# Optimization experiments

Measured on AMD Instinct MI355X. Metric: run time of the kernel, lower is better.

Reference implementation:

```python
import jax, jax.numpy as jnp
import numpy as np

N, E, NFEAT, NHID = 50000, 800000, 256, 128
EPS = 1e-5


def setup_inputs() -> dict:
    key = jax.random.key(0)
    ks = jax.random.split(key, 12)
    s = 0.05
    return {
        "x": jax.random.normal(ks[0], (N, NFEAT), jnp.float32),
        "adj": jax.random.randint(ks[1], (2, E), 0, N, jnp.int32),
        "features": jax.random.uniform(ks[2], (E,), jnp.float32),
        "W_in": jax.random.normal(ks[3], (NHID, NFEAT), jnp.float32) * s,
        "b_in": jnp.zeros((NHID,), jnp.float32),
        "W1_rel": jax.random.normal(ks[4], (NHID, NHID), jnp.float32) * s,
        "b1_rel": jnp.zeros((NHID,), jnp.float32),
        "W1_root": jax.random.normal(ks[5], (NHID, NHID), jnp.float32) * s,
        "W2_rel": jax.random.normal(ks[6], (NHID, NHID), jnp.float32) * s,
        "b2_rel": jnp.zeros((NHID,), jnp.float32),
        "W2_root": jax.random.normal(ks[7], (NHID, NHID), jnp.float32) * s,
        "gamma": jnp.ones((NHID,), jnp.float32),
        "beta": jnp.zeros((NHID,), jnp.float32),
    }


def _graph_conv(h, src, dst, ew, W_rel, b_rel, W_root):
    # torch_geometric GraphConv (aggr='add'):
    #   out_i = W_rel @ (sum_{j->i} e_ji * h_j) + b_rel + W_root @ h_i
    msg = h[src] * ew[:, None]                       # [E, NHID] gather
    agg = jax.ops.segment_sum(msg, dst, num_segments=N)  # [N, NHID] scatter-add
    return agg @ W_rel.T + b_rel + h @ W_root.T


def _batch_norm(h, gamma, beta):
    mu = h.mean(axis=0)
    var = h.var(axis=0)
    return (h - mu) * jax.lax.rsqrt(var + EPS) * gamma + beta


def reference(x, adj, features, W_in, b_in, W1_rel, b1_rel, W1_root,
              W2_rel, b2_rel, W2_root, gamma, beta):
    src, dst = adj[0], adj[1]
    h = jax.nn.relu(x @ W_in.T + b_in)               # linear_in + relu (dropout=identity in eval)
    h = _graph_conv(h, src, dst, features, W1_rel, b1_rel, W1_root)
    h = jax.nn.relu(_batch_norm(h, gamma, beta))     # batch1 + relu
    h = _graph_conv(h, src, dst, features, W2_rel, b2_rel, W2_root)
    return _batch_norm(h, gamma, beta)               # batch1 reused (per source)
```

## Files before the change

### kernel.cpp

```cpp
#include <hip/hip_runtime.h>
#include <hip/hip_bf16.h>

#define NNODES 50000
#define NEDGES 800000
#define NF 256
#define NH 128
#define BN_EPS 1e-5f
#define MTILES (NNODES / 16)
#define GEMM_BLOCKS 512
#define NBUCKETS 196
#define BCAP 4608
#define SCAT_BLOCKS ((NEDGES + 2047) / 2048)

typedef __attribute__((ext_vector_type(8))) __bf16 bf16x8;
typedef __attribute__((ext_vector_type(4))) float floatx4;

__device__ __forceinline__ __hip_bfloat16 f2bf(float f) { return __float2bfloat16(f); }
__device__ __forceinline__ float bits2f(unsigned short b) {
    union { unsigned u; float f; } u; u.u = ((unsigned)b) << 16; return u.f;
}

__device__ __forceinline__ bf16x8 cvt8(const float* __restrict__ p) {
    floatx4 a0 = *(const floatx4*)p;
    floatx4 a1 = *(const floatx4*)(p + 4);
    bf16x8 r;
    r[0] = (__bf16)a0[0]; r[1] = (__bf16)a0[1]; r[2] = (__bf16)a0[2]; r[3] = (__bf16)a0[3];
    r[4] = (__bf16)a1[0]; r[5] = (__bf16)a1[1]; r[6] = (__bf16)a1[2]; r[7] = (__bf16)a1[3];
    return r;
}

__global__ __launch_bounds__(256) void convert_w_kernel(
    const float* __restrict__ W_in, const float* __restrict__ W1r,
    const float* __restrict__ W1o, const float* __restrict__ W2r,
    const float* __restrict__ W2o, __hip_bfloat16* __restrict__ wbf,
    int* __restrict__ gcursor, float* __restrict__ st1, float* __restrict__ st2)
{
    const int i = blockIdx.x * 256 + threadIdx.x;
    if (blockIdx.x == 0 && threadIdx.x < NBUCKETS)
        gcursor[threadIdx.x] = threadIdx.x * BCAP;
    if (blockIdx.x == 1) { st1[threadIdx.x] = 0.f; st2[threadIdx.x] = 0.f; }
    const float* src; int off;
    if (i < 32768)      { src = W_in; off = i; }
    else if (i < 49152) { src = W1r;  off = i - 32768; }
    else if (i < 65536) { src = W1o;  off = i - 49152; }
    else if (i < 81920) { src = W2r;  off = i - 65536; }
    else                { src = W2o;  off = i - 81920; }
    wbf[i] = f2bf(src[off]);
}

__global__ __launch_bounds__(256) void bucket_scatter_kernel(
    const int* __restrict__ adj, const float* __restrict__ ew,
    int* __restrict__ gcursor, uint2* __restrict__ pairbuf,
    unsigned char* __restrict__ nodebuf)
{
    __shared__ int cnt[NBUCKETS];
    __shared__ int base[NBUCKETS];
    const int tid = threadIdx.x;
    if (tid < NBUCKETS) cnt[tid] = 0;
    __syncthreads();
    const int e0 = blockIdx.x * 2048;
    #pragma unroll
    for (int i = 0; i < 8; ++i) {
        const int e = e0 + i * 256 + tid;
        if (e < NEDGES) atomicAdd(&cnt[adj[NEDGES + e] >> 8], 1);
    }
    __syncthreads();
    if (tid < NBUCKETS) {
        base[tid] = atomicAdd(&gcursor[tid], cnt[tid]);
        cnt[tid] = 0;
    }
    __syncthreads();
    #pragma unroll
    for (int i = 0; i < 8; ++i) {
        const int e = e0 + i * 256 + tid;
        if (e >= NEDGES) continue;
        const int dst = adj[NEDGES + e];
        const int b = dst >> 8;
        const int off = atomicAdd(&cnt[b], 1);
        const int slot = base[b] + off;
        if (slot < (b + 1) * BCAP) {
            pairbuf[slot] = make_uint2((unsigned)adj[e], __float_as_uint(ew[e]));
            nodebuf[slot] = (unsigned char)(dst & 255);
        }
    }
}

__global__ __launch_bounds__(256) void bucket_sort_kernel(
    const int* __restrict__ gcursor, const uint2* __restrict__ pairbuf,
    const unsigned char* __restrict__ nodebuf, uint2* __restrict__ sorted,
    int* __restrict__ rowptr, int* __restrict__ rowend)
{
    const int b = blockIdx.x;
    const int tid = threadIdx.x;
    const int capbase = b * BCAP;
    int n = gcursor[b] - capbase;
    if (n > BCAP) n = BCAP;

    __shared__ int cnt[256];
    __shared__ int s[256];
    cnt[tid] = 0;
    __syncthreads();
    for (int j = tid; j < n; j += 256)
        atomicAdd(&cnt[nodebuf[capbase + j]], 1);
    __syncthreads();
    const int v = cnt[tid];
    s[tid] = v;
    __syncthreads();
    for (int off = 1; off < 256; off <<= 1) {
        const int t = (tid >= off) ? s[tid - off] : 0;
        __syncthreads();
        s[tid] += t;
        __syncthreads();
    }
    const int excl = s[tid] - v;
    const int node = b * 256 + tid;
    if (node < NNODES) {
        rowptr[node] = capbase + excl;
        rowend[node] = capbase + excl + v;
    }
    cnt[tid] = excl;
    __syncthreads();
    for (int j = tid; j < n; j += 256) {
        const int nd = nodebuf[capbase + j];
        const int pos = atomicAdd(&cnt[nd], 1);
        sorted[capbase + pos] = pairbuf[capbase + j];
    }
}

__global__ __launch_bounds__(256, 2) void gemm_in_kernel(
    const float* __restrict__ X, const __hip_bfloat16* __restrict__ W,
    const float* __restrict__ bias, __hip_bfloat16* __restrict__ out)
{
    const int waveG = blockIdx.x * 4 + (threadIdx.x >> 6);
    const int lane = threadIdx.x & 63;
    const int half = waveG & 1;
    const int ar = lane & 15;
    const int q  = lane >> 4;

    bf16x8 bw[4][8];
    float bv[4];
    #pragma unroll
    for (int t = 0; t < 4; ++t) {
        const int row = half * 64 + t * 16 + ar;
        bv[t] = bias[row];
        #pragma unroll
        for (int k = 0; k < 8; ++k)
            bw[t][k] = *(const bf16x8*)(W + (size_t)row * NF + k * 32 + q * 8);
    }

    for (int strip = waveG >> 1; strip < MTILES; strip += GEMM_BLOCKS * 2) {
        const int m0 = strip << 4;
        floatx4 acc[4] = {};
        #pragma unroll
        for (int k = 0; k < 8; ++k) {
            const bf16x8 a = cvt8(X + (size_t)(m0 + ar) * NF + k * 32 + q * 8);
            #pragma unroll
            for (int t = 0; t < 4; ++t)
                acc[t] = __builtin_amdgcn_mfma_f32_16x16x32_bf16(a, bw[t][k], acc[t], 0, 0, 0);
        }
        #pragma unroll
        for (int t = 0; t < 4; ++t) {
            const int col = half * 64 + t * 16 + ar;
            #pragma unroll
            for (int r = 0; r < 4; ++r) {
                const float v = fmaxf(acc[t][r] + bv[t], 0.f);
                out[(size_t)(m0 + q * 4 + r) * NH + col] = f2bf(v);
            }
        }
    }
}

__global__ __launch_bounds__(256) void gather_kernel(
    const uint2* __restrict__ sorted, const int* __restrict__ rowptr,
    const int* __restrict__ rowend,
    const __hip_bfloat16* __restrict__ h, __hip_bfloat16* __restrict__ agg)
{
    const int node = blockIdx.x * 4 + (threadIdx.x >> 6);
    if (node >= NNODES) return;
    const int lane = threadIdx.x & 63;
    const int beg = rowptr[node];
    const int end = rowend[node];
    const unsigned short* hb = (const unsigned short*)h;

    float a0[8] = {}, a1[8] = {};

    int j = beg;
    if ((j & 1) && j < end) {
        const uint2 ev = sorted[j++];
        const float w = __uint_as_float(ev.y);
        const unsigned raw = *(const unsigned*)(hb + (size_t)ev.x * NH + lane * 2);
        a0[0] += w * bits2f((unsigned short)(raw & 0xffffu));
        a1[0] += w * bits2f((unsigned short)(raw >> 16));
    }
    for (; j + 8 <= end; j += 8) {
        const uint4 e01 = *(const uint4*)(sorted + j);
        const uint4 e23 = *(const uint4*)(sorted + j + 2);
        const uint4 e45 = *(const uint4*)(sorted + j + 4);
        const uint4 e67 = *(const uint4*)(sorted + j + 6);
        const unsigned r0 = *(const unsigned*)(hb + (size_t)e01.x * NH + lane * 2);
        const unsigned r1 = *(const unsigned*)(hb + (size_t)e01.z * NH + lane * 2);
        const unsigned r2 = *(const unsigned*)(hb + (size_t)e23.x * NH + lane * 2);
        const unsigned r3 = *(const unsigned*)(hb + (size_t)e23.z * NH + lane * 2);
        const unsigned r4 = *(const unsigned*)(hb + (size_t)e45.x * NH + lane * 2);
        const unsigned r5 = *(const unsigned*)(hb + (size_t)e45.z * NH + lane * 2);
        const unsigned r6 = *(const unsigned*)(hb + (size_t)e67.x * NH + lane * 2);
        const unsigned r7 = *(const unsigned*)(hb + (size_t)e67.z * NH + lane * 2);
        const float w0 = __uint_as_float(e01.y), w1 = __uint_as_float(e01.w);
        const float w2 = __uint_as_float(e23.y), w3 = __uint_as_float(e23.w);
        const float w4 = __uint_as_float(e45.y), w5 = __uint_as_float(e45.w);
        const float w6 = __uint_as_float(e67.y), w7 = __uint_as_float(e67.w);
        a0[0] += w0 * bits2f((unsigned short)(r0 & 0xffffu));
        a1[0] += w0 * bits2f((unsigned short)(r0 >> 16));
        a0[1] += w1 * bits2f((unsigned short)(r1 & 0xffffu));
        a1[1] += w1 * bits2f((unsigned short)(r1 >> 16));
        a0[2] += w2 * bits2f((unsigned short)(r2 & 0xffffu));
        a1[2] += w2 * bits2f((unsigned short)(r2 >> 16));
        a0[3] += w3 * bits2f((unsigned short)(r3 & 0xffffu));
        a1[3] += w3 * bits2f((unsigned short)(r3 >> 16));
        a0[4] += w4 * bits2f((unsigned short)(r4 & 0xffffu));
        a1[4] += w4 * bits2f((unsigned short)(r4 >> 16));
        a0[5] += w5 * bits2f((unsigned short)(r5 & 0xffffu));
        a1[5] += w5 * bits2f((unsigned short)(r5 >> 16));
        a0[6] += w6 * bits2f((unsigned short)(r6 & 0xffffu));
        a1[6] += w6 * bits2f((unsigned short)(r6 >> 16));
        a0[7] += w7 * bits2f((unsigned short)(r7 & 0xffffu));
        a1[7] += w7 * bits2f((unsigned short)(r7 >> 16));
    }
    for (; j + 2 <= end; j += 2) {
        const uint4 e01 = *(const uint4*)(sorted + j);
        const unsigned r0 = *(const unsigned*)(hb + (size_t)e01.x * NH + lane * 2);
        const unsigned r1 = *(const unsigned*)(hb + (size_t)e01.z * NH + lane * 2);
        const float w0 = __uint_as_float(e01.y), w1 = __uint_as_float(e01.w);
        a0[0] += w0 * bits2f((unsigned short)(r0 & 0xffffu));
        a1[0] += w0 * bits2f((unsigned short)(r0 >> 16));
        a0[1] += w1 * bits2f((unsigned short)(r1 & 0xffffu));
        a1[1] += w1 * bits2f((unsigned short)(r1 >> 16));
    }
    if (j < end) {
        const uint2 ev = sorted[j];
        const float w = __uint_as_float(ev.y);
        const unsigned raw = *(const unsigned*)(hb + (size_t)ev.x * NH + lane * 2);
        a0[0] += w * bits2f((unsigned short)(raw & 0xffffu));
        a1[0] += w * bits2f((unsigned short)(raw >> 16));
    }
    const float f0 = ((a0[0] + a0[1]) + (a0[2] + a0[3])) + ((a0[4] + a0[5]) + (a0[6] + a0[7]));
    const float f1 = ((a1[0] + a1[1]) + (a1[2] + a1[3])) + ((a1[4] + a1[5]) + (a1[6] + a1[7]));
    unsigned o = ((unsigned)__bfloat16_as_ushort(f2bf(f1)) << 16) |
                 (unsigned)__bfloat16_as_ushort(f2bf(f0));
    *(unsigned*)((unsigned short*)agg + (size_t)node * NH + lane * 2) = o;
}

__global__ __launch_bounds__(256, 2) void gemm_conv_kernel(
    const __hip_bfloat16* __restrict__ agg, const __hip_bfloat16* __restrict__ h,
    const __hip_bfloat16* __restrict__ Wrel, const __hip_bfloat16* __restrict__ Wroot,
    const float* __restrict__ bias, float* __restrict__ out,
    float* __restrict__ stats)
{
    const int waveG = blockIdx.x * 4 + (threadIdx.x >> 6);
    const int lane = threadIdx.x & 63;
    const int half = waveG & 1;
    const int ar = lane & 15;
    const int q  = lane >> 4;

    bf16x8 brel[4][4], brt[4][4];
    float bv[4];
    #pragma unroll
    for (int t = 0; t < 4; ++t) {
        const int row = half * 64 + t * 16 + ar;
        bv[t] = bias[row];
        #pragma unroll
        for (int k = 0; k < 4; ++k) {
            brel[t][k] = *(const bf16x8*)(Wrel + (size_t)row * NH + k * 32 + q * 8);
            brt[t][k]  = *(const bf16x8*)(Wroot + (size_t)row * NH + k * 32 + q * 8);
        }
    }

    float s1[4] = {}, s2[4] = {};

    for (int strip = waveG >> 1; strip < MTILES; strip += GEMM_BLOCKS * 2) {
        const int m0 = strip << 4;
        floatx4 acc[4] = {};
        #pragma unroll
        for (int k = 0; k < 4; ++k) {
            const bf16x8 a = *(const bf16x8*)(agg + (size_t)(m0 + ar) * NH + k * 32 + q * 8);
            #pragma unroll
            for (int t = 0; t < 4; ++t)
                acc[t] = __builtin_amdgcn_mfma_f32_16x16x32_bf16(a, brel[t][k], acc[t], 0, 0, 0);
        }
        #pragma unroll
        for (int k = 0; k < 4; ++k) {
            const bf16x8 a = *(const bf16x8*)(h + (size_t)(m0 + ar) * NH + k * 32 + q * 8);
            #pragma unroll
            for (int t = 0; t < 4; ++t)
                acc[t] = __builtin_amdgcn_mfma_f32_16x16x32_bf16(a, brt[t][k], acc[t], 0, 0, 0);
        }
        #pragma unroll
        for (int t = 0; t < 4; ++t) {
            const int col = half * 64 + t * 16 + ar;
            #pragma unroll
            for (int r = 0; r < 4; ++r) {
                const float v = acc[t][r] + bv[t];
                out[(size_t)(m0 + q * 4 + r) * NH + col] = v;
                s1[t] += v; s2[t] += v * v;
            }
        }
    }

    __shared__ float sst[256];
    sst[threadIdx.x] = 0.f;
    __syncthreads();
    #pragma unroll
    for (int t = 0; t < 4; ++t) {
        float a = s1[t], b = s2[t];
        a += __shfl_xor(a, 16, 64); a += __shfl_xor(a, 32, 64);
        b += __shfl_xor(b, 16, 64); b += __shfl_xor(b, 32, 64);
        if (q == 0) {
            const int col = half * 64 + t * 16 + ar;
            atomicAdd(&sst[col], a);
            atomicAdd(&sst[128 + col], b);
        }
    }
    __syncthreads();
    unsafeAtomicAdd(&stats[threadIdx.x], sst[threadIdx.x]);
}

__global__ __launch_bounds__(256) void bn_relu_bf16_kernel(
    const float* __restrict__ t, const float* __restrict__ stats,
    const float* __restrict__ gamma, const float* __restrict__ beta,
    __hip_bfloat16* __restrict__ out)
{
    const size_t i = (size_t)blockIdx.x * blockDim.x + threadIdx.x;
    const int c = (int)(i & (NH - 1));
    const float inv_n = 1.0f / (float)NNODES;
    const float mu = stats[c] * inv_n;
    const float var = stats[128 + c] * inv_n - mu * mu;
    const float rs = rsqrtf(var + BN_EPS);
    float v = (t[i] - mu) * rs * gamma[c] + beta[c];
    out[i] = f2bf(fmaxf(v, 0.f));
}

__global__ __launch_bounds__(256) void bn_f32_kernel(
    const float* __restrict__ t, const float* __restrict__ stats,
    const float* __restrict__ gamma, const float* __restrict__ beta,
    float* __restrict__ out)
{
    const size_t i = (size_t)blockIdx.x * blockDim.x + threadIdx.x;
    const int c = (int)(i & (NH - 1));
    const float inv_n = 1.0f / (float)NNODES;
    const float mu = stats[c] * inv_n;
    const float var = stats[128 + c] * inv_n - mu * mu;
    const float rs = rsqrtf(var + BN_EPS);
    out[i] = (t[i] - mu) * rs * gamma[c] + beta[c];
}


extern "C" void kernel_launch(void* const* d_in, const int* in_sizes, int n_in,
                              void* d_out, int out_size, void* d_ws, size_t ws_size,
                              hipStream_t stream)
{
    const float* x    = (const float*)d_in[0];
    const int*   adj  = (const int*)d_in[1];
    const float* ew   = (const float*)d_in[2];
    const float* W_in = (const float*)d_in[3];
    const float* b_in = (const float*)d_in[4];
    const float* W1r  = (const float*)d_in[5];
    const float* b1   = (const float*)d_in[6];
    const float* W1o  = (const float*)d_in[7];
    const float* W2r  = (const float*)d_in[8];
    const float* b2   = (const float*)d_in[9];
    const float* W2o  = (const float*)d_in[10];
    const float* gmm  = (const float*)d_in[11];
    const float* bta  = (const float*)d_in[12];
    float* out = (float*)d_out;
    float* t   = (float*)d_out;

    char* ws = (char*)d_ws;
    __hip_bfloat16* h0  = (__hip_bfloat16*)ws; ws += (size_t)NNODES * NH * 2;
    __hip_bfloat16* h1  = (__hip_bfloat16*)ws; ws += (size_t)NNODES * NH * 2;
    __hip_bfloat16* agg = (__hip_bfloat16*)ws; ws += (size_t)NNODES * NH * 2;
    uint2*          sorted  = (uint2*)ws;      ws += (size_t)NBUCKETS * BCAP * 8;
    uint2*          pairbuf = (uint2*)ws;      ws += (size_t)NBUCKETS * BCAP * 8;
    unsigned char*  nodebuf = (unsigned char*)ws; ws += (size_t)NBUCKETS * BCAP;
    int*            rowptr  = (int*)ws;        ws += NNODES * 4;
    int*            rowend  = (int*)ws;        ws += NNODES * 4;
    int*            gcursor = (int*)ws;        ws += ((NBUCKETS + 3) & ~3) * 4;
    __hip_bfloat16* wbf     = (__hip_bfloat16*)ws; ws += 98304 * 2;
    float*          st1     = (float*)ws;      ws += 256 * 4;
    float*          st2     = (float*)ws;      ws += 256 * 4;

    const __hip_bfloat16* Wb_in = wbf;
    const __hip_bfloat16* Wb1r  = wbf + 32768;
    const __hip_bfloat16* Wb1o  = wbf + 49152;
    const __hip_bfloat16* Wb2r  = wbf + 65536;
    const __hip_bfloat16* Wb2o  = wbf + 81920;

    const int node_blocks = (NNODES + 3) / 4;
    const int bn_blocks   = (NNODES * NH) / 256;

    convert_w_kernel<<<98304 / 256, 256, 0, stream>>>(W_in, W1r, W1o, W2r, W2o,
                                                      wbf, gcursor, st1, st2);
    bucket_scatter_kernel<<<SCAT_BLOCKS, 256, 0, stream>>>(adj, ew, gcursor, pairbuf, nodebuf);
    bucket_sort_kernel<<<NBUCKETS, 256, 0, stream>>>(gcursor, pairbuf, nodebuf,
                                                     sorted, rowptr, rowend);

    gemm_in_kernel<<<GEMM_BLOCKS, 256, 0, stream>>>(x, Wb_in, b_in, h0);
    gather_kernel<<<node_blocks, 256, 0, stream>>>(sorted, rowptr, rowend, h0, agg);
    gemm_conv_kernel<<<GEMM_BLOCKS, 256, 0, stream>>>(agg, h0, Wb1r, Wb1o, b1, t, st1);
    bn_relu_bf16_kernel<<<bn_blocks, 256, 0, stream>>>(t, st1, gmm, bta, h1);

    gather_kernel<<<node_blocks, 256, 0, stream>>>(sorted, rowptr, rowend, h1, agg);
    gemm_conv_kernel<<<GEMM_BLOCKS, 256, 0, stream>>>(agg, h1, Wb2r, Wb2o, b2, t, st2);
    bn_f32_kernel<<<bn_blocks, 256, 0, stream>>>(t, st2, gmm, bta, out);
}
```

Baseline: 327.0 us.

## Fuse bucket scatter with input GEMM, retile GEMMs, store pre-BN output in bf16

Merges the edge bucket-scatter kernel and the input linear GEMM into one launch, with extra blocks taking the GEMM role so the two independent stages can run concurrently. Both GEMM kernels are retiled so each block's four waves split the 128 output columns of a single 16-row strip (32 columns per wave). This halves the weight registers each wave holds and the launch bounds are raised to 4 blocks per CU. The pre-batchnorm conv output is now written to a bf16 workspace buffer instead of fp32 in the output buffer, halving that traffic at some cost in precision before the final normalization.

```diff
diff --git a/kernel.cpp b/kernel.cpp
--- a/kernel.cpp
+++ b/kernel.cpp
@@ -48,39 +48,80 @@
     wbf[i] = f2bf(src[off]);
 }
 
-__global__ __launch_bounds__(256) void bucket_scatter_kernel(
+__global__ __launch_bounds__(256, 4) void scatter_gemm_in_kernel(
     const int* __restrict__ adj, const float* __restrict__ ew,
     int* __restrict__ gcursor, uint2* __restrict__ pairbuf,
-    unsigned char* __restrict__ nodebuf)
+    unsigned char* __restrict__ nodebuf,
+    const float* __restrict__ X, const __hip_bfloat16* __restrict__ W,
+    const float* __restrict__ bias, __hip_bfloat16* __restrict__ out)
 {
     __shared__ int cnt[NBUCKETS];
     __shared__ int base[NBUCKETS];
     const int tid = threadIdx.x;
-    if (tid < NBUCKETS) cnt[tid] = 0;
-    __syncthreads();
-    const int e0 = blockIdx.x * 2048;
-    #pragma unroll
-    for (int i = 0; i < 8; ++i) {
-        const int e = e0 + i * 256 + tid;
-        if (e < NEDGES) atomicAdd(&cnt[adj[NEDGES + e] >> 8], 1);
-    }
-    __syncthreads();
-    if (tid < NBUCKETS) {
-        base[tid] = atomicAdd(&gcursor[tid], cnt[tid]);
-        cnt[tid] = 0;
-    }
-    __syncthreads();
-    #pragma unroll
-    for (int i = 0; i < 8; ++i) {
-        const int e = e0 + i * 256 + tid;
-        if (e >= NEDGES) continue;
-        const int dst = adj[NEDGES + e];
-        const int b = dst >> 8;
-        const int off = atomicAdd(&cnt[b], 1);
-        const int slot = base[b] + off;
-        if (slot < (b + 1) * BCAP) {
-            pairbuf[slot] = make_uint2((unsigned)adj[e], __float_as_uint(ew[e]));
-            nodebuf[slot] = (unsigned char)(dst & 255);
+
+    if (blockIdx.x < SCAT_BLOCKS) {
+        if (tid < NBUCKETS) cnt[tid] = 0;
+        __syncthreads();
+        const int e0 = blockIdx.x * 2048;
+        #pragma unroll
+        for (int i = 0; i < 8; ++i) {
+            const int e = e0 + i * 256 + tid;
+            if (e < NEDGES) atomicAdd(&cnt[adj[NEDGES + e] >> 8], 1);
+        }
+        __syncthreads();
+        if (tid < NBUCKETS) {
+            base[tid] = atomicAdd(&gcursor[tid], cnt[tid]);
+            cnt[tid] = 0;
+        }
+        __syncthreads();
+        #pragma unroll
+        for (int i = 0; i < 8; ++i) {
+            const int e = e0 + i * 256 + tid;
+            if (e >= NEDGES) continue;
+            const int dst = adj[NEDGES + e];
+            const int b = dst >> 8;
+            const int off = atomicAdd(&cnt[b], 1);
+            const int slot = base[b] + off;
+            if (slot < (b + 1) * BCAP) {
+                pairbuf[slot] = make_uint2((unsigned)adj[e], __float_as_uint(ew[e]));
+                nodebuf[slot] = (unsigned char)(dst & 255);
+            }
+        }
+    } else {
+        const int q4   = tid >> 6;
+        const int lane = tid & 63;
+        const int ar = lane & 15;
+        const int q  = lane >> 4;
+
+        bf16x8 bw[2][8];
+        float bv[2];
+        #pragma unroll
+        for (int tt = 0; tt < 2; ++tt) {
+            const int row = q4 * 32 + tt * 16 + ar;
+            bv[tt] = bias[row];
+            #pragma unroll
+            for (int k = 0; k < 8; ++k)
+                bw[tt][k] = *(const bf16x8*)(W + (size_t)row * NF + k * 32 + q * 8);
+        }
+
+        for (int s = blockIdx.x - SCAT_BLOCKS; s < MTILES; s += GEMM_BLOCKS) {
+            const int m0 = s << 4;
+            floatx4 acc[2] = {};
+            #pragma unroll
+            for (int k = 0; k < 8; ++k) {
+                const bf16x8 a = cvt8(X + (size_t)(m0 + ar) * NF + k * 32 + q * 8);
+                acc[0] = __builtin_amdgcn_mfma_f32_16x16x32_bf16(a, bw[0][k], acc[0], 0, 0, 0);
+                acc[1] = __builtin_amdgcn_mfma_f32_16x16x32_bf16(a, bw[1][k], acc[1], 0, 0, 0);
+            }
+            #pragma unroll
+            for (int tt = 0; tt < 2; ++tt) {
+                const int col = q4 * 32 + tt * 16 + ar;
+                #pragma unroll
+                for (int r = 0; r < 4; ++r) {
+                    const float v = fmaxf(acc[tt][r] + bv[tt], 0.f);
+                    out[(size_t)(m0 + q * 4 + r) * NH + col] = f2bf(v);
+                }
+            }
         }
     }
 }
@@ -124,49 +165,6 @@
         const int nd = nodebuf[capbase + j];
         const int pos = atomicAdd(&cnt[nd], 1);
         sorted[capbase + pos] = pairbuf[capbase + j];
-    }
-}
-
-__global__ __launch_bounds__(256, 2) void gemm_in_kernel(
-    const float* __restrict__ X, const __hip_bfloat16* __restrict__ W,
-    const float* __restrict__ bias, __hip_bfloat16* __restrict__ out)
-{
-    const int waveG = blockIdx.x * 4 + (threadIdx.x >> 6);
-    const int lane = threadIdx.x & 63;
-    const int half = waveG & 1;
-    const int ar = lane & 15;
-    const int q  = lane >> 4;
-
-    bf16x8 bw[4][8];
-    float bv[4];
-    #pragma unroll
-    for (int t = 0; t < 4; ++t) {
-        const int row = half * 64 + t * 16 + ar;
-        bv[t] = bias[row];
-        #pragma unroll
-        for (int k = 0; k < 8; ++k)
-            bw[t][k] = *(const bf16x8*)(W + (size_t)row * NF + k * 32 + q * 8);
-    }
-
-    for (int strip = waveG >> 1; strip < MTILES; strip += GEMM_BLOCKS * 2) {
-        const int m0 = strip << 4;
-        floatx4 acc[4] = {};
-        #pragma unroll
-        for (int k = 0; k < 8; ++k) {
-            const bf16x8 a = cvt8(X + (size_t)(m0 + ar) * NF + k * 32 + q * 8);
-            #pragma unroll
-            for (int t = 0; t < 4; ++t)
-                acc[t] = __builtin_amdgcn_mfma_f32_16x16x32_bf16(a, bw[t][k], acc[t], 0, 0, 0);
-        }
-        #pragma unroll
-        for (int t = 0; t < 4; ++t) {
-            const int col = half * 64 + t * 16 + ar;
-            #pragma unroll
-            for (int r = 0; r < 4; ++r) {
-                const float v = fmaxf(acc[t][r] + bv[t], 0.f);
-                out[(size_t)(m0 + q * 4 + r) * NH + col] = f2bf(v);
-            }
-        }
     }
 }
 
@@ -250,58 +248,55 @@
     *(unsigned*)((unsigned short*)agg + (size_t)node * NH + lane * 2) = o;
 }
 
-__global__ __launch_bounds__(256, 2) void gemm_conv_kernel(
+__global__ __launch_bounds__(256, 4) void gemm_conv_kernel(
     const __hip_bfloat16* __restrict__ agg, const __hip_bfloat16* __restrict__ h,
     const __hip_bfloat16* __restrict__ Wrel, const __hip_bfloat16* __restrict__ Wroot,
-    const float* __restrict__ bias, float* __restrict__ out,
+    const float* __restrict__ bias, __hip_bfloat16* __restrict__ out,
     float* __restrict__ stats)
 {
-    const int waveG = blockIdx.x * 4 + (threadIdx.x >> 6);
+    const int q4   = threadIdx.x >> 6;
     const int lane = threadIdx.x & 63;
-    const int half = waveG & 1;
     const int ar = lane & 15;
     const int q  = lane >> 4;
 
-    bf16x8 brel[4][4], brt[4][4];
-    float bv[4];
+    bf16x8 brel[2][4], brt[2][4];
+    float bv[2];
     #pragma unroll
-    for (int t = 0; t < 4; ++t) {
-        const int row = half * 64 + t * 16 + ar;
-        bv[t] = bias[row];
+    for (int tt = 0; tt < 2; ++tt) {
+        const int row = q4 * 32 + tt * 16 + ar;
+        bv[tt] = bias[row];
         #pragma unroll
         for (int k = 0; k < 4; ++k) {
-            brel[t][k] = *(const bf16x8*)(Wrel + (size_t)row * NH + k * 32 + q * 8);
-            brt[t][k]  = *(const bf16x8*)(Wroot + (size_t)row * NH + k * 32 + q * 8);
-        }
-    }
-
-    float s1[4] = {}, s2[4] = {};
-
-    for (int strip = waveG >> 1; strip < MTILES; strip += GEMM_BLOCKS * 2) {
-        const int m0 = strip << 4;
-        floatx4 acc[4] = {};
+            brel[tt][k] = *(const bf16x8*)(Wrel + (size_t)row * NH + k * 32 + q * 8);
+            brt[tt][k]  = *(const bf16x8*)(Wroot + (size_t)row * NH + k * 32 + q * 8);
+        }
+    }
+
+    float s1[2] = {}, s2[2] = {};
+
+    for (int s = blockIdx.x; s < MTILES; s += GEMM_BLOCKS) {
+        const int m0 = s << 4;
+        floatx4 acc[2] = {};
         #pragma unroll
         for (int k = 0; k < 4; ++k) {
             const bf16x8 a = *(const bf16x8*)(agg + (size_t)(m0 + ar) * NH + k * 32 + q * 8);
-            #pragma unroll
-            for (int t = 0; t < 4; ++t)
-                acc[t] = __builtin_amdgcn_mfma_f32_16x16x32_bf16(a, brel[t][k], acc[t], 0, 0, 0);
+            acc[0] = __builtin_amdgcn_mfma_f32_16x16x32_bf16(a, brel[0][k], acc[0], 0, 0, 0);
+            acc[1] = __builtin_amdgcn_mfma_f32_16x16x32_bf16(a, brel[1][k], acc[1], 0, 0, 0);
         }
         #pragma unroll
         for (int k = 0; k < 4; ++k) {
             const bf16x8 a = *(const bf16x8*)(h + (size_t)(m0 + ar) * NH + k * 32 + q * 8);
-            #pragma unroll
-            for (int t = 0; t < 4; ++t)
-                acc[t] = __builtin_amdgcn_mfma_f32_16x16x32_bf16(a, brt[t][k], acc[t], 0, 0, 0);
-        }
-        #pragma unroll
-        for (int t = 0; t < 4; ++t) {
-            const int col = half * 64 + t * 16 + ar;
+            acc[0] = __builtin_amdgcn_mfma_f32_16x16x32_bf16(a, brt[0][k], acc[0], 0, 0, 0);
+            acc[1] = __builtin_amdgcn_mfma_f32_16x16x32_bf16(a, brt[1][k], acc[1], 0, 0, 0);
+        }
+        #pragma unroll
+        for (int tt = 0; tt < 2; ++tt) {
+            const int col = q4 * 32 + tt * 16 + ar;
             #pragma unroll
             for (int r = 0; r < 4; ++r) {
-                const float v = acc[t][r] + bv[t];
-                out[(size_t)(m0 + q * 4 + r) * NH + col] = v;
-                s1[t] += v; s2[t] += v * v;
+                const float v = acc[tt][r] + bv[tt];
+                out[(size_t)(m0 + q * 4 + r) * NH + col] = f2bf(v);
+                s1[tt] += v; s2[tt] += v * v;
             }
         }
     }
@@ -310,12 +305,12 @@
     sst[threadIdx.x] = 0.f;
     __syncthreads();
     #pragma unroll
-    for (int t = 0; t < 4; ++t) {
-        float a = s1[t], b = s2[t];
+    for (int tt = 0; tt < 2; ++tt) {
+        float a = s1[tt], b = s2[tt];
         a += __shfl_xor(a, 16, 64); a += __shfl_xor(a, 32, 64);
         b += __shfl_xor(b, 16, 64); b += __shfl_xor(b, 32, 64);
         if (q == 0) {
-            const int col = half * 64 + t * 16 + ar;
+            const int col = q4 * 32 + tt * 16 + ar;
             atomicAdd(&sst[col], a);
             atomicAdd(&sst[128 + col], b);
         }
@@ -325,7 +320,7 @@
 }
 
 __global__ __launch_bounds__(256) void bn_relu_bf16_kernel(
-    const float* __restrict__ t, const float* __restrict__ stats,
+    const __hip_bfloat16* __restrict__ t, const float* __restrict__ stats,
     const float* __restrict__ gamma, const float* __restrict__ beta,
     __hip_bfloat16* __restrict__ out)
 {
@@ -335,12 +330,12 @@
     const float mu = stats[c] * inv_n;
     const float var = stats[128 + c] * inv_n - mu * mu;
     const float rs = rsqrtf(var + BN_EPS);
-    float v = (t[i] - mu) * rs * gamma[c] + beta[c];
+    float v = (__bfloat162float(t[i]) - mu) * rs * gamma[c] + beta[c];
     out[i] = f2bf(fmaxf(v, 0.f));
 }
 
 __global__ __launch_bounds__(256) void bn_f32_kernel(
-    const float* __restrict__ t, const float* __restrict__ stats,
+    const __hip_bfloat16* __restrict__ t, const float* __restrict__ stats,
     const float* __restrict__ gamma, const float* __restrict__ beta,
     float* __restrict__ out)
 {
@@ -350,7 +345,7 @@
     const float mu = stats[c] * inv_n;
     const float var = stats[128 + c] * inv_n - mu * mu;
     const float rs = rsqrtf(var + BN_EPS);
-    out[i] = (t[i] - mu) * rs * gamma[c] + beta[c];
+    out[i] = (__bfloat162float(t[i]) - mu) * rs * gamma[c] + beta[c];
 }
 
 
@@ -372,12 +367,12 @@
     const float* gmm  = (const float*)d_in[11];
     const float* bta  = (const float*)d_in[12];
     float* out = (float*)d_out;
-    float* t   = (float*)d_out;
 
     char* ws = (char*)d_ws;
     __hip_bfloat16* h0  = (__hip_bfloat16*)ws; ws += (size_t)NNODES * NH * 2;
     __hip_bfloat16* h1  = (__hip_bfloat16*)ws; ws += (size_t)NNODES * NH * 2;
     __hip_bfloat16* agg = (__hip_bfloat16*)ws; ws += (size_t)NNODES * NH * 2;
+    __hip_bfloat16* t   = (__hip_bfloat16*)ws; ws += (size_t)NNODES * NH * 2;
     uint2*          sorted  = (uint2*)ws;      ws += (size_t)NBUCKETS * BCAP * 8;
     uint2*          pairbuf = (uint2*)ws;      ws += (size_t)NBUCKETS * BCAP * 8;
     unsigned char*  nodebuf = (unsigned char*)ws; ws += (size_t)NBUCKETS * BCAP;
@@ -399,11 +394,11 @@
 
     convert_w_kernel<<<98304 / 256, 256, 0, stream>>>(W_in, W1r, W1o, W2r, W2o,
                                                       wbf, gcursor, st1, st2);
-    bucket_scatter_kernel<<<SCAT_BLOCKS, 256, 0, stream>>>(adj, ew, gcursor, pairbuf, nodebuf);
+    scatter_gemm_in_kernel<<<SCAT_BLOCKS + GEMM_BLOCKS, 256, 0, stream>>>(
+        adj, ew, gcursor, pairbuf, nodebuf, x, Wb_in, b_in, h0);
     bucket_sort_kernel<<<NBUCKETS, 256, 0, stream>>>(gcursor, pairbuf, nodebuf,
                                                      sorted, rowptr, rowend);
 
-    gemm_in_kernel<<<GEMM_BLOCKS, 256, 0, stream>>>(x, Wb_in, b_in, h0);
     gather_kernel<<<node_blocks, 256, 0, stream>>>(sorted, rowptr, rowend, h0, agg);
     gemm_conv_kernel<<<GEMM_BLOCKS, 256, 0, stream>>>(agg, h0, Wb1r, Wb1o, b1, t, st1);
     bn_relu_bf16_kernel<<<bn_blocks, 256, 0, stream>>>(t, st1, gmm, bta, h1);
```

New measurement: 334.1 us. +2.2%, slower.
